# Performance work log

Measured on AMD Instinct MI355X. Metric: run time of the kernel, lower is better.

## Reference

```python
import jax, jax.numpy as jnp
import numpy as np

EPS = 1e-5
N = 384
CZ = 128  # pair channels (c_z)
CH = 128  # hidden channels (c_hidden)


def _layer_norm(x, w, b):
    m = jnp.mean(x, axis=-1, keepdims=True)
    v = jnp.mean(jnp.square(x - m), axis=-1, keepdims=True)
    return (x - m) * jax.lax.rsqrt(v + EPS) * w + b


def setup_inputs() -> dict:
    key = jax.random.key(0)
    ks = jax.random.split(key, 8)
    s = 0.02  # weight init scale
    return {
        "z": jax.random.normal(ks[0], (1, N, N, CZ), jnp.float32),
        "ln_in_w": jnp.ones((2, CZ), jnp.float32),
        "ln_in_b": jnp.zeros((2, CZ), jnp.float32),
        "w_ag": jax.random.normal(ks[1], (2, CZ, CH), jnp.float32) * s,
        "b_ag": jnp.zeros((2, CH), jnp.float32),
        "w_ap": jax.random.normal(ks[2], (2, CZ, CH), jnp.float32) * s,
        "b_ap": jnp.zeros((2, CH), jnp.float32),
        "w_bg": jax.random.normal(ks[3], (2, CZ, CH), jnp.float32) * s,
        "b_bg": jnp.zeros((2, CH), jnp.float32),
        "w_bp": jax.random.normal(ks[4], (2, CZ, CH), jnp.float32) * s,
        "b_bp": jnp.zeros((2, CH), jnp.float32),
        "ln_out_w": jnp.ones((2, CH), jnp.float32),
        "ln_out_b": jnp.zeros((2, CH), jnp.float32),
        "w_z": jax.random.normal(ks[5], (2, CH, CZ), jnp.float32) * s,
        "b_z": jnp.zeros((2, CZ), jnp.float32),
        "w_g": jax.random.normal(ks[6], (2, CZ, CZ), jnp.float32) * s,
        "b_g": jnp.zeros((2, CZ), jnp.float32),
    }


def _tri_mul(z, outgoing, ln_in_w, ln_in_b, w_ag, b_ag, w_ap, b_ap,
             w_bg, b_bg, w_bp, b_bp, ln_out_w, ln_out_b, w_z, b_z, w_g, b_g):
    zn = _layer_norm(z, ln_in_w, ln_in_b)                      # [1,N,N,CZ]
    a = jax.nn.sigmoid(zn @ w_ag + b_ag) * (zn @ w_ap + b_ap)  # [1,N,N,CH]
    b = jax.nn.sigmoid(zn @ w_bg + b_bg) * (zn @ w_bp + b_bp)  # [1,N,N,CH]
    if outgoing:
        # p[i,k,c] = sum_j a[i,j,c] * b[k,j,c]
        p = jnp.einsum('bijc,bkjc->bikc', a, b)
    else:
        # p[i,k,c] = sum_j a[j,i,c] * b[j,k,c]
        p = jnp.einsum('bjic,bjkc->bikc', a, b)
    p = _layer_norm(p, ln_out_w, ln_out_b) @ w_z + b_z         # [1,N,N,CZ]
    g = jax.nn.sigmoid(zn @ w_g + b_g)
    return p * g


def reference(z, ln_in_w, ln_in_b, w_ag, b_ag, w_ap, b_ap, w_bg, b_bg,
              w_bp, b_bp, ln_out_w, ln_out_b, w_z, b_z, w_g, b_g):
    # idx 0: TriMulOut (outgoing=True), idx 1: TriMulIn (outgoing=False)
    for idx, outgoing in enumerate((True, False)):
        z = z + _tri_mul(z, outgoing,
                         ln_in_w[idx], ln_in_b[idx],
                         w_ag[idx], b_ag[idx], w_ap[idx], b_ap[idx],
                         w_bg[idx], b_bg[idx], w_bp[idx], b_bp[idx],
                         ln_out_w[idx], ln_out_b[idx],
                         w_z[idx], b_z[idx], w_g[idx], b_g[idx])
    return z
```

## Files before the change

kernel.cpp:

```cpp
#include <hip/hip_runtime.h>


constexpr int NS = 384;
constexpr int NN = NS * NS;

using bf16x8 = __attribute__((ext_vector_type(8))) __bf16;
using bf16x4 = __attribute__((ext_vector_type(4))) __bf16;
using f32x4  = __attribute__((ext_vector_type(4))) float;

__device__ inline void load16_to_lds(const __bf16* g, __bf16* lds) {
  auto* gp = reinterpret_cast<const __attribute__((address_space(1))) unsigned int*>(
      reinterpret_cast<uintptr_t>(g));
  auto* lp = reinterpret_cast<__attribute__((address_space(3))) unsigned int*>(
      reinterpret_cast<uintptr_t>(lds));
  __builtin_amdgcn_global_load_lds(gp, lp, 16, 0, 0);
}

__device__ inline float fast_sigmoid(float x) {
  float d = 1.0f + __expf(-x);
  float r;
  asm("v_rcp_f32 %0, %1" : "=v"(r) : "v"(d));
  return r;
}

__global__ __launch_bounds__(256) void prep_weights(
    const float* __restrict__ w_ag, const float* __restrict__ w_ap,
    const float* __restrict__ w_bg, const float* __restrict__ w_bp,
    const float* __restrict__ w_g,  const float* __restrict__ w_z,
    __bf16* __restrict__ wsw)
{
  int gid  = blockIdx.x * 256 + threadIdx.x;
  int mat  = gid >> 11;
  int slot = gid & 2047;
  int lane = slot & 63;
  int tb   = (slot >> 6) & 7;
  int s    = slot >> 9;
  int pass = mat / 6, which = mat % 6;
  const float* W;
  switch (which) {
    case 0: W = w_ag; break; case 1: W = w_ap; break; case 2: W = w_bg; break;
    case 3: W = w_bp; break; case 4: W = w_g;  break; default: W = w_z;
  }
  W += pass * 16384;
  int n0 = tb * 16 + (lane & 15);
  int k0 = s * 32 + (lane >> 4) * 8;
  __bf16* dst = wsw + ((size_t)mat * 2048 + slot) * 8;
#pragma unroll
  for (int j = 0; j < 8; ++j) dst[j] = (__bf16)W[(k0 + j) * 128 + n0];
}

template <typename DstRow>
__device__ inline void ln_row_interleaved(const float* __restrict__ zrow, int q,
                                          const float* __restrict__ lnw,
                                          const float* __restrict__ lnb,
                                          DstRow dstrow)
{
  const float4* zp = (const float4*)zrow;
  float4 v[8];
#pragma unroll
  for (int u = 0; u < 8; ++u) v[u] = zp[u * 4 + q];
  __builtin_amdgcn_sched_barrier(0);
  float s1 = 0.f, s2 = 0.f;
#pragma unroll
  for (int u = 0; u < 8; ++u) {
    float4 t = v[u];
    s1 += t.x + t.y + t.z + t.w;
    s2 += t.x * t.x + t.y * t.y + t.z * t.z + t.w * t.w;
  }
  s1 += __shfl_xor(s1, 1); s2 += __shfl_xor(s2, 1);
  s1 += __shfl_xor(s1, 2); s2 += __shfl_xor(s2, 2);
  float mean = s1 * (1.0f / 128.0f);
  float var  = s2 * (1.0f / 128.0f) - mean * mean;
  float rstd = rsqrtf(var + 1e-5f);
#pragma unroll
  for (int u = 0; u < 8; ++u) {
    int c0 = u * 16 + q * 4;
    float4 t  = v[u];
    float4 w4 = *(const float4*)(lnw + c0);
    float4 b4 = *(const float4*)(lnb + c0);
    dstrow[c0 + 0] = (__bf16)((t.x - mean) * rstd * w4.x + b4.x);
    dstrow[c0 + 1] = (__bf16)((t.y - mean) * rstd * w4.y + b4.y);
    dstrow[c0 + 2] = (__bf16)((t.z - mean) * rstd * w4.z + b4.z);
    dstrow[c0 + 3] = (__bf16)((t.w - mean) * rstd * w4.w + b4.w);
  }
}

__global__ __launch_bounds__(256) void proj_kernel(
    const float* __restrict__ zsrc, const float* __restrict__ lnw, const float* __restrict__ lnb,
    const __bf16* __restrict__ wsw5,
    const float* __restrict__ bag, const float* __restrict__ bap,
    const float* __restrict__ bbg, const float* __restrict__ bbp,
    __bf16* __restrict__ a_t, __bf16* __restrict__ b_t, int mode)
{
  __shared__ __bf16 zn[64][136];
  int tid = threadIdx.x;
  int rb = 0, r2 = 0;
  size_t pstart = 0;
  if (mode == 0) pstart = (size_t)blockIdx.x * 64;
  else { rb = blockIdx.x / NS; r2 = blockIdx.x % NS; }

  const int wv = tid >> 6;
  const int lane = tid & 63;
  const int lm = lane & 15;
  const int lq = lane >> 4;

  {
    int row = tid >> 2, q = tid & 3;
    size_t zoff = (mode == 0) ? (pstart + row) * 128
                              : ((size_t)(64 * rb + row) * NS + r2) * 128;
    ln_row_interleaved(zsrc + zoff, q, lnw, lnb, &zn[row][0]);
  }
  __syncthreads();

  const size_t wposbase = (mode == 0) ? pstart : ((size_t)r2 * NS + 64 * rb);

#pragma unroll
  for (int set = 0; set < 4; ++set) {
    const int grp = set >> 1, mbi = set & 1;
    const int mb = 2 * wv + mbi;
    const __bf16* wG = wsw5 + (size_t)(2 * grp) * 16384;
    const __bf16* wP = wG + 16384;
    bf16x8 fG[4], fP[4];
#pragma unroll
    for (int s = 0; s < 4; ++s) {
      fG[s] = *(const bf16x8*)(wG + ((size_t)((s * 8 + mb) * 64 + lane)) * 8);
      fP[s] = *(const bf16x8*)(wP + ((size_t)((s * 8 + mb) * 64 + lane)) * 8);
    }
    const int cc = 16 * mb + lm;
    const float bG = (grp ? bbg : bag)[cc];
    const float bP = (grp ? bbp : bap)[cc];
    __bf16* dst = grp ? b_t : a_t;
    __bf16* drow = dst + (size_t)cc * NN + wposbase + 4 * lq;
#pragma unroll
    for (int nt = 0; nt < 4; ++nt) {
      bf16x8 z0 = *(const bf16x8*)(&zn[16 * nt + lm][8 * lq]);
      bf16x8 z1 = *(const bf16x8*)(&zn[16 * nt + lm][32 + 8 * lq]);
      bf16x8 z2 = *(const bf16x8*)(&zn[16 * nt + lm][64 + 8 * lq]);
      bf16x8 z3 = *(const bf16x8*)(&zn[16 * nt + lm][96 + 8 * lq]);
      f32x4 acc0 = {0.f, 0.f, 0.f, 0.f}, acc1 = {0.f, 0.f, 0.f, 0.f};
      acc0 = __builtin_amdgcn_mfma_f32_16x16x32_bf16(z0, fG[0], acc0, 0, 0, 0);
      acc1 = __builtin_amdgcn_mfma_f32_16x16x32_bf16(z0, fP[0], acc1, 0, 0, 0);
      acc0 = __builtin_amdgcn_mfma_f32_16x16x32_bf16(z1, fG[1], acc0, 0, 0, 0);
      acc1 = __builtin_amdgcn_mfma_f32_16x16x32_bf16(z1, fP[1], acc1, 0, 0, 0);
      acc0 = __builtin_amdgcn_mfma_f32_16x16x32_bf16(z2, fG[2], acc0, 0, 0, 0);
      acc1 = __builtin_amdgcn_mfma_f32_16x16x32_bf16(z2, fP[2], acc1, 0, 0, 0);
      acc0 = __builtin_amdgcn_mfma_f32_16x16x32_bf16(z3, fG[3], acc0, 0, 0, 0);
      acc1 = __builtin_amdgcn_mfma_f32_16x16x32_bf16(z3, fP[3], acc1, 0, 0, 0);
      bf16x4 pk;
#pragma unroll
      for (int r = 0; r < 4; ++r) {
        float xg = acc0[r] + bG;
        float xp = acc1[r] + bP;
        pk[r] = (__bf16)(xp * fast_sigmoid(xg));
      }
      *(bf16x4*)(drow + 16 * nt) = pk;
    }
  }
}

__global__ __launch_bounds__(256) void tri_kernel(
    const __bf16* __restrict__ a_t, const __bf16* __restrict__ b_t, __bf16* __restrict__ p_t)
{
  __shared__ __bf16 As[128 * 64];
  __shared__ __bf16 Bs[128 * 64];
  int lin = blockIdx.x;
  int xcd = lin & 7;
  int loc = lin >> 3;
  int cq  = loc / 9;
  int tile = loc - 9 * cq;
  int c  = (xcd << 4) | cq;
  int i0 = (tile % 3) * 128, k0 = (tile / 3) * 128;
  const __bf16* Ab = a_t + (size_t)c * NN;
  const __bf16* Bb = b_t + (size_t)c * NN;
  int tid = threadIdx.x, wv = tid >> 6, lane = tid & 63;
  int lm = lane & 15, lq = lane >> 4;
  int lrow = lane >> 3;
  int lsl  = lane & 7;
  int lch  = lsl ^ lrow;
  f32x4 acc[4][4];
#pragma unroll
  for (int mi = 0; mi < 4; ++mi)
#pragma unroll
    for (int ni = 0; ni < 4; ++ni) acc[mi][ni] = {0.f, 0.f, 0.f, 0.f};
  const int rowA_half = 64 * (wv & 1), colB_half = 64 * (wv >> 1);

  for (int kk = 0; kk < 384; kk += 64) {
    __syncthreads();
#pragma unroll
    for (int v = 0; v < 4; ++v) {
      int rgrp = 4 * wv + v;
      int r = 8 * rgrp + lrow;
      load16_to_lds(Ab + (size_t)(i0 + r) * NS + kk + lch * 8, As + rgrp * 512);
      load16_to_lds(Bb + (size_t)(k0 + r) * NS + kk + lch * 8, Bs + rgrp * 512);
    }
    __syncthreads();
#pragma unroll
    for (int s = 0; s < 2; ++s) {
      bf16x8 bfr[4], afr[4];
#pragma unroll
      for (int ni = 0; ni < 4; ++ni)
        bfr[ni] = *(const bf16x8*)(Bs + (colB_half + 16 * ni + lm) * 64 +
                                   ((4 * s + lq) ^ (lm & 7)) * 8);
#pragma unroll
      for (int mi = 0; mi < 4; ++mi)
        afr[mi] = *(const bf16x8*)(As + (rowA_half + 16 * mi + lm) * 64 +
                                   ((4 * s + lq) ^ (lm & 7)) * 8);
#pragma unroll
      for (int mi = 0; mi < 4; ++mi)
#pragma unroll
        for (int ni = 0; ni < 4; ++ni)
          acc[mi][ni] = __builtin_amdgcn_mfma_f32_16x16x32_bf16(afr[mi], bfr[ni], acc[mi][ni], 0, 0, 0);
    }
  }
#pragma unroll
  for (int mi = 0; mi < 4; ++mi)
#pragma unroll
    for (int ni = 0; ni < 4; ++ni)
#pragma unroll
      for (int r = 0; r < 4; ++r) {
        int row = i0 + rowA_half + 16 * mi + 4 * lq + r;
        int col = k0 + colB_half + 16 * ni + lm;
        p_t[(size_t)c * NN + (size_t)row * NS + col] = (__bf16)acc[mi][ni][r];
      }
}

__global__ __launch_bounds__(256) void out_kernel(
    const __bf16* __restrict__ p_t,
    const float* __restrict__ z_in, float* __restrict__ z_out,
    const float* __restrict__ lniw, const float* __restrict__ lnib,
    const float* __restrict__ lnow, const float* __restrict__ lnob,
    const __bf16* __restrict__ wz, const float* __restrict__ bz,
    const __bf16* __restrict__ wg, const float* __restrict__ bg)
{
  __shared__ __bf16 pl[64][136];
  __shared__ __bf16 znl[64][136];
  int tid = threadIdx.x;
  size_t base = (size_t)blockIdx.x * 64;

  {
    int row = tid >> 2, q = tid & 3;
    ln_row_interleaved(z_in + (base + row) * 128, q, lniw, lnib, &znl[row][0]);
  }

  {
    int c2 = tid >> 1, hf = tid & 1;
    const __bf16* src = p_t + (size_t)c2 * NN + base + hf * 32;
    bf16x8 v0 = ((const bf16x8*)src)[0];
    bf16x8 v1 = ((const bf16x8*)src)[1];
    bf16x8 v2 = ((const bf16x8*)src)[2];
    bf16x8 v3 = ((const bf16x8*)src)[3];
#pragma unroll
    for (int j = 0; j < 8; ++j) pl[hf * 32 + j][c2] = v0[j];
#pragma unroll
    for (int j = 0; j < 8; ++j) pl[hf * 32 + 8 + j][c2] = v1[j];
#pragma unroll
    for (int j = 0; j < 8; ++j) pl[hf * 32 + 16 + j][c2] = v2[j];
#pragma unroll
    for (int j = 0; j < 8; ++j) pl[hf * 32 + 24 + j][c2] = v3[j];
  }
  __syncthreads();

  {
    int row = tid >> 2, q = tid & 3;
    bf16x8 pv[4];
#pragma unroll
    for (int s = 0; s < 4; ++s) pv[s] = *(const bf16x8*)(&pl[row][q * 32 + 8 * s]);
    float s1 = 0.f, s2 = 0.f;
#pragma unroll
    for (int s = 0; s < 4; ++s)
#pragma unroll
      for (int j = 0; j < 8; ++j) { float f = (float)pv[s][j]; s1 += f; s2 += f * f; }
    s1 += __shfl_xor(s1, 1); s2 += __shfl_xor(s2, 1);
    s1 += __shfl_xor(s1, 2); s2 += __shfl_xor(s2, 2);
    float mean = s1 * (1.0f / 128.0f);
    float var  = s2 * (1.0f / 128.0f) - mean * mean;
    float rstd = rsqrtf(var + 1e-5f);
#pragma unroll
    for (int s = 0; s < 4; ++s) {
#pragma unroll
      for (int j = 0; j < 8; ++j) {
        int cc = q * 32 + 8 * s + j;
        float f = ((float)pv[s][j] - mean) * rstd * lnow[cc] + lnob[cc];
        pv[s][j] = (__bf16)f;
      }
      *(bf16x8*)(&pl[row][q * 32 + 8 * s]) = pv[s];
    }
  }
  __syncthreads();

  int wv = tid >> 6, lane = tid & 63, lm = lane & 15, lq = lane >> 4;
  bf16x8 wzf[2][4], wgf[2][4];
  float bzv[2], bgv[2];
#pragma unroll
  for (int nbi = 0; nbi < 2; ++nbi) {
    int nb = 2 * wv + nbi;
    bzv[nbi] = bz[16 * nb + lm];
    bgv[nbi] = bg[16 * nb + lm];
#pragma unroll
    for (int s = 0; s < 4; ++s) {
      wzf[nbi][s] = *(const bf16x8*)(wz + ((size_t)((s * 8 + nb) * 64 + lane)) * 8);
      wgf[nbi][s] = *(const bf16x8*)(wg + ((size_t)((s * 8 + nb) * 64 + lane)) * 8);
    }
  }
#pragma unroll
  for (int mt = 0; mt < 4; ++mt) {
    bf16x8 af[4], zf[4];
#pragma unroll
    for (int s = 0; s < 4; ++s) {
      af[s] = *(const bf16x8*)(&pl[16 * mt + lm][32 * s + 8 * lq]);
      zf[s] = *(const bf16x8*)(&znl[16 * mt + lm][32 * s + 8 * lq]);
    }
#pragma unroll
    for (int nbi = 0; nbi < 2; ++nbi) {
      f32x4 accp = {0.f, 0.f, 0.f, 0.f};
      f32x4 accg = {0.f, 0.f, 0.f, 0.f};
#pragma unroll
      for (int s = 0; s < 4; ++s) {
        accp = __builtin_amdgcn_mfma_f32_16x16x32_bf16(af[s], wzf[nbi][s], accp, 0, 0, 0);
        accg = __builtin_amdgcn_mfma_f32_16x16x32_bf16(zf[s], wgf[nbi][s], accg, 0, 0, 0);
      }
      int cz = 16 * (2 * wv + nbi) + lm;
#pragma unroll
      for (int r = 0; r < 4; ++r) {
        int pos = 16 * mt + 4 * lq + r;
        size_t idx = (base + pos) * 128 + cz;
        float gv  = fast_sigmoid(accg[r] + bgv[nbi]);
        float res = (accp[r] + bzv[nbi]) * gv + z_in[idx];
        z_out[idx] = res;
      }
    }
  }
}

extern "C" void kernel_launch(void* const* d_in, const int* in_sizes, int n_in,
                              void* d_out, int out_size, void* d_ws, size_t ws_size,
                              hipStream_t stream) {
  (void)in_sizes; (void)n_in; (void)out_size; (void)ws_size;
  const float* z        = (const float*)d_in[0];
  const float* ln_in_w  = (const float*)d_in[1];
  const float* ln_in_b  = (const float*)d_in[2];
  const float* w_ag     = (const float*)d_in[3];
  const float* b_ag     = (const float*)d_in[4];
  const float* w_ap     = (const float*)d_in[5];
  const float* b_ap     = (const float*)d_in[6];
  const float* w_bg     = (const float*)d_in[7];
  const float* b_bg     = (const float*)d_in[8];
  const float* w_bp     = (const float*)d_in[9];
  const float* b_bp     = (const float*)d_in[10];
  const float* ln_out_w = (const float*)d_in[11];
  const float* ln_out_b = (const float*)d_in[12];
  const float* w_z      = (const float*)d_in[13];
  const float* b_z      = (const float*)d_in[14];
  const float* w_g      = (const float*)d_in[15];
  const float* b_g      = (const float*)d_in[16];
  float* out = (float*)d_out;

  __bf16* wsw = (__bf16*)d_ws;
  __bf16* a_t = wsw + 12 * 16384;
  __bf16* b_t = a_t + (size_t)NN * 128;
  __bf16* p_t = b_t + (size_t)NN * 128;

  prep_weights<<<96, 256, 0, stream>>>(w_ag, w_ap, w_bg, w_bp, w_g, w_z, wsw);

  for (int idx = 0; idx < 2; ++idx) {
    const float* zsrc = (idx == 0) ? z : out;
    const __bf16* wsw5 = wsw + (size_t)idx * 6 * 16384;
    proj_kernel<<<2304, 256, 0, stream>>>(
        zsrc, ln_in_w + idx * 128, ln_in_b + idx * 128, wsw5,
        b_ag + idx * 128, b_ap + idx * 128, b_bg + idx * 128, b_bp + idx * 128,
        a_t, b_t, idx);
    tri_kernel<<<1152, 256, 0, stream>>>(a_t, b_t, p_t);
    out_kernel<<<2304, 256, 0, stream>>>(
        p_t, zsrc, out,
        ln_in_w + idx * 128, ln_in_b + idx * 128,
        ln_out_w + idx * 128, ln_out_b + idx * 128,
        wsw5 + 5 * 16384, b_z + idx * 128,
        wsw5 + 4 * 16384, b_g + idx * 128);
  }
}
```

Baseline: 376.5 us.

## Double proj_kernel row tile and skew LDS transpose in out_kernel

proj_kernel now processes 128 positions per block instead of 64, so each block loads its weight fragments once for twice as many rows and the grid is halved. out_kernel's transposed load of p_t into LDS is reorganised so lanes read 16-byte chunks across channels and write to LDS in a rotated order, meant to reduce bank conflicts. The larger tile doubles LDS use in proj_kernel and may lower occupancy.

```diff
diff --git a/kernel.cpp b/kernel.cpp
--- a/kernel.cpp
+++ b/kernel.cpp
@@ -92,11 +92,11 @@
     const float* __restrict__ bbg, const float* __restrict__ bbp,
     __bf16* __restrict__ a_t, __bf16* __restrict__ b_t, int mode)
 {
-  __shared__ __bf16 zn[64][136];
+  __shared__ __bf16 zn[128][136];
   int tid = threadIdx.x;
   int rb = 0, r2 = 0;
   size_t pstart = 0;
-  if (mode == 0) pstart = (size_t)blockIdx.x * 64;
+  if (mode == 0) pstart = (size_t)blockIdx.x * 128;
   else { rb = blockIdx.x / NS; r2 = blockIdx.x % NS; }
 
   const int wv = tid >> 6;
@@ -106,13 +106,17 @@
 
   {
     int row = tid >> 2, q = tid & 3;
-    size_t zoff = (mode == 0) ? (pstart + row) * 128
-                              : ((size_t)(64 * rb + row) * NS + r2) * 128;
-    ln_row_interleaved(zsrc + zoff, q, lnw, lnb, &zn[row][0]);
+#pragma unroll
+    for (int half = 0; half < 2; ++half) {
+      int r = row + 64 * half;
+      size_t zoff = (mode == 0) ? (pstart + r) * 128
+                                : ((size_t)(128 * rb + r) * NS + r2) * 128;
+      ln_row_interleaved(zsrc + zoff, q, lnw, lnb, &zn[r][0]);
+    }
   }
   __syncthreads();
 
-  const size_t wposbase = (mode == 0) ? pstart : ((size_t)r2 * NS + 64 * rb);
+  const size_t wposbase = (mode == 0) ? pstart : ((size_t)r2 * NS + 128 * rb);
 
 #pragma unroll
   for (int set = 0; set < 4; ++set) {
@@ -132,7 +136,7 @@
     __bf16* dst = grp ? b_t : a_t;
     __bf16* drow = dst + (size_t)cc * NN + wposbase + 4 * lq;
 #pragma unroll
-    for (int nt = 0; nt < 4; ++nt) {
+    for (int nt = 0; nt < 8; ++nt) {
       bf16x8 z0 = *(const bf16x8*)(&zn[16 * nt + lm][8 * lq]);
       bf16x8 z1 = *(const bf16x8*)(&zn[16 * nt + lm][32 + 8 * lq]);
       bf16x8 z2 = *(const bf16x8*)(&zn[16 * nt + lm][64 + 8 * lq]);
@@ -243,20 +247,19 @@
   }
 
   {
-    int c2 = tid >> 1, hf = tid & 1;
-    const __bf16* src = p_t + (size_t)c2 * NN + base + hf * 32;
-    bf16x8 v0 = ((const bf16x8*)src)[0];
-    bf16x8 v1 = ((const bf16x8*)src)[1];
-    bf16x8 v2 = ((const bf16x8*)src)[2];
-    bf16x8 v3 = ((const bf16x8*)src)[3];
-#pragma unroll
-    for (int j = 0; j < 8; ++j) pl[hf * 32 + j][c2] = v0[j];
-#pragma unroll
-    for (int j = 0; j < 8; ++j) pl[hf * 32 + 8 + j][c2] = v1[j];
-#pragma unroll
-    for (int j = 0; j < 8; ++j) pl[hf * 32 + 16 + j][c2] = v2[j];
-#pragma unroll
-    for (int j = 0; j < 8; ++j) pl[hf * 32 + 24 + j][c2] = v3[j];
+    int w = tid >> 6, l = tid & 63;
+    int s = l >> 3, rl = l & 7;
+    const __bf16* srcb = p_t + base + s * 8;
+#pragma unroll
+    for (int j = 0; j < 4; ++j) {
+      int ch = 32 * w + 8 * j + rl;
+      bf16x8 v = *(const bf16x8*)(srcb + (size_t)ch * NN);
+#pragma unroll
+      for (int t = 0; t < 8; ++t) {
+        int k = (s + t) & 7;
+        pl[8 * s + k][ch] = v[k];
+      }
+    }
   }
   __syncthreads();
 
@@ -365,7 +368,7 @@
   for (int idx = 0; idx < 2; ++idx) {
     const float* zsrc = (idx == 0) ? z : out;
     const __bf16* wsw5 = wsw + (size_t)idx * 6 * 16384;
-    proj_kernel<<<2304, 256, 0, stream>>>(
+    proj_kernel<<<1152, 256, 0, stream>>>(
         zsrc, ln_in_w + idx * 128, ln_in_b + idx * 128, wsw5,
         b_ag + idx * 128, b_ap + idx * 128, b_bg + idx * 128, b_bp + idx * 128,
         a_t, b_t, idx);
```

Result: slower. 384.4 us (+2.1%).

## Drop LDS staging in tri_kernel and double proj_kernel rows per block

Applied to the files above, without the earlier changes.

The triangle-multiply GEMM kernel now loads MFMA fragments straight from global memory into registers instead of staging 64-wide K tiles through swizzled LDS with barriers. Removing the barriers and LDS round trip is meant to cut synchronisation stalls, and the kernel relies on L2/L1 caching for the reuse across waves. The projection kernel now processes 128 rows per block with half the grid, amortising the weight-fragment loads across more rows. The cost is uncoalesced, redundant global fragment loads in tri_kernel and fewer blocks in proj_kernel.

```diff
diff --git a/kernel.cpp b/kernel.cpp
--- a/kernel.cpp
+++ b/kernel.cpp
@@ -7,14 +7,6 @@
 using bf16x8 = __attribute__((ext_vector_type(8))) __bf16;
 using bf16x4 = __attribute__((ext_vector_type(4))) __bf16;
 using f32x4  = __attribute__((ext_vector_type(4))) float;
-
-__device__ inline void load16_to_lds(const __bf16* g, __bf16* lds) {
-  auto* gp = reinterpret_cast<const __attribute__((address_space(1))) unsigned int*>(
-      reinterpret_cast<uintptr_t>(g));
-  auto* lp = reinterpret_cast<__attribute__((address_space(3))) unsigned int*>(
-      reinterpret_cast<uintptr_t>(lds));
-  __builtin_amdgcn_global_load_lds(gp, lp, 16, 0, 0);
-}
 
 __device__ inline float fast_sigmoid(float x) {
   float d = 1.0f + __expf(-x);
@@ -92,11 +84,11 @@
     const float* __restrict__ bbg, const float* __restrict__ bbp,
     __bf16* __restrict__ a_t, __bf16* __restrict__ b_t, int mode)
 {
-  __shared__ __bf16 zn[64][136];
+  __shared__ __bf16 zn[128][136];
   int tid = threadIdx.x;
   int rb = 0, r2 = 0;
   size_t pstart = 0;
-  if (mode == 0) pstart = (size_t)blockIdx.x * 64;
+  if (mode == 0) pstart = (size_t)blockIdx.x * 128;
   else { rb = blockIdx.x / NS; r2 = blockIdx.x % NS; }
 
   const int wv = tid >> 6;
@@ -106,13 +98,17 @@
 
   {
     int row = tid >> 2, q = tid & 3;
-    size_t zoff = (mode == 0) ? (pstart + row) * 128
-                              : ((size_t)(64 * rb + row) * NS + r2) * 128;
-    ln_row_interleaved(zsrc + zoff, q, lnw, lnb, &zn[row][0]);
+#pragma unroll
+    for (int half = 0; half < 2; ++half) {
+      int r = row + 64 * half;
+      size_t zoff = (mode == 0) ? (pstart + r) * 128
+                                : ((size_t)(128 * rb + r) * NS + r2) * 128;
+      ln_row_interleaved(zsrc + zoff, q, lnw, lnb, &zn[r][0]);
+    }
   }
   __syncthreads();
 
-  const size_t wposbase = (mode == 0) ? pstart : ((size_t)r2 * NS + 64 * rb);
+  const size_t wposbase = (mode == 0) ? pstart : ((size_t)r2 * NS + 128 * rb);
 
 #pragma unroll
   for (int set = 0; set < 4; ++set) {
@@ -132,7 +128,7 @@
     __bf16* dst = grp ? b_t : a_t;
     __bf16* drow = dst + (size_t)cc * NN + wposbase + 4 * lq;
 #pragma unroll
-    for (int nt = 0; nt < 4; ++nt) {
+    for (int nt = 0; nt < 8; ++nt) {
       bf16x8 z0 = *(const bf16x8*)(&zn[16 * nt + lm][8 * lq]);
       bf16x8 z1 = *(const bf16x8*)(&zn[16 * nt + lm][32 + 8 * lq]);
       bf16x8 z2 = *(const bf16x8*)(&zn[16 * nt + lm][64 + 8 * lq]);
@@ -161,8 +157,6 @@
 __global__ __launch_bounds__(256) void tri_kernel(
     const __bf16* __restrict__ a_t, const __bf16* __restrict__ b_t, __bf16* __restrict__ p_t)
 {
-  __shared__ __bf16 As[128 * 64];
-  __shared__ __bf16 Bs[128 * 64];
   int lin = blockIdx.x;
   int xcd = lin & 7;
   int loc = lin >> 3;
@@ -170,47 +164,32 @@
   int tile = loc - 9 * cq;
   int c  = (xcd << 4) | cq;
   int i0 = (tile % 3) * 128, k0 = (tile / 3) * 128;
-  const __bf16* Ab = a_t + (size_t)c * NN;
-  const __bf16* Bb = b_t + (size_t)c * NN;
   int tid = threadIdx.x, wv = tid >> 6, lane = tid & 63;
   int lm = lane & 15, lq = lane >> 4;
-  int lrow = lane >> 3;
-  int lsl  = lane & 7;
-  int lch  = lsl ^ lrow;
+  const int rowA = i0 + 64 * (wv & 1);
+  const int rowB = k0 + 64 * (wv >> 1);
+  const __bf16* Ab = a_t + (size_t)c * NN + (size_t)(rowA + lm) * NS + 8 * lq;
+  const __bf16* Bb = b_t + (size_t)c * NN + (size_t)(rowB + lm) * NS + 8 * lq;
   f32x4 acc[4][4];
 #pragma unroll
   for (int mi = 0; mi < 4; ++mi)
 #pragma unroll
     for (int ni = 0; ni < 4; ++ni) acc[mi][ni] = {0.f, 0.f, 0.f, 0.f};
-  const int rowA_half = 64 * (wv & 1), colB_half = 64 * (wv >> 1);
-
-  for (int kk = 0; kk < 384; kk += 64) {
-    __syncthreads();
-#pragma unroll
-    for (int v = 0; v < 4; ++v) {
-      int rgrp = 4 * wv + v;
-      int r = 8 * rgrp + lrow;
-      load16_to_lds(Ab + (size_t)(i0 + r) * NS + kk + lch * 8, As + rgrp * 512);
-      load16_to_lds(Bb + (size_t)(k0 + r) * NS + kk + lch * 8, Bs + rgrp * 512);
-    }
-    __syncthreads();
-#pragma unroll
-    for (int s = 0; s < 2; ++s) {
-      bf16x8 bfr[4], afr[4];
+
+#pragma unroll 2
+  for (int s = 0; s < 12; ++s) {
+    bf16x8 afr[4], bfr[4];
+#pragma unroll
+    for (int mi = 0; mi < 4; ++mi)
+      afr[mi] = *(const bf16x8*)(Ab + (size_t)(16 * mi) * NS + 32 * s);
+#pragma unroll
+    for (int ni = 0; ni < 4; ++ni)
+      bfr[ni] = *(const bf16x8*)(Bb + (size_t)(16 * ni) * NS + 32 * s);
+#pragma unroll
+    for (int mi = 0; mi < 4; ++mi)
 #pragma unroll
       for (int ni = 0; ni < 4; ++ni)
-        bfr[ni] = *(const bf16x8*)(Bs + (colB_half + 16 * ni + lm) * 64 +
-                                   ((4 * s + lq) ^ (lm & 7)) * 8);
-#pragma unroll
-      for (int mi = 0; mi < 4; ++mi)
-        afr[mi] = *(const bf16x8*)(As + (rowA_half + 16 * mi + lm) * 64 +
-                                   ((4 * s + lq) ^ (lm & 7)) * 8);
-#pragma unroll
-      for (int mi = 0; mi < 4; ++mi)
-#pragma unroll
-        for (int ni = 0; ni < 4; ++ni)
-          acc[mi][ni] = __builtin_amdgcn_mfma_f32_16x16x32_bf16(afr[mi], bfr[ni], acc[mi][ni], 0, 0, 0);
-    }
+        acc[mi][ni] = __builtin_amdgcn_mfma_f32_16x16x32_bf16(afr[mi], bfr[ni], acc[mi][ni], 0, 0, 0);
   }
 #pragma unroll
   for (int mi = 0; mi < 4; ++mi)
@@ -218,8 +197,8 @@
     for (int ni = 0; ni < 4; ++ni)
 #pragma unroll
       for (int r = 0; r < 4; ++r) {
-        int row = i0 + rowA_half + 16 * mi + 4 * lq + r;
-        int col = k0 + colB_half + 16 * ni + lm;
+        int row = rowA + 16 * mi + 4 * lq + r;
+        int col = rowB + 16 * ni + lm;
         p_t[(size_t)c * NN + (size_t)row * NS + col] = (__bf16)acc[mi][ni][r];
       }
 }
@@ -365,7 +344,7 @@
   for (int idx = 0; idx < 2; ++idx) {
     const float* zsrc = (idx == 0) ? z : out;
     const __bf16* wsw5 = wsw + (size_t)idx * 6 * 16384;
-    proj_kernel<<<2304, 256, 0, stream>>>(
+    proj_kernel<<<1152, 256, 0, stream>>>(
         zsrc, ln_in_w + idx * 128, ln_in_b + idx * 128, wsw5,
         b_ag + idx * 128, b_ap + idx * 128, b_bg + idx * 128, b_bp + idx * 128,
         a_t, b_t, idx);
```

Result: slower. 436.3 us (+15.9%).
